# Kernel optimization log

Measured on AMD Instinct MI355X. Metric: run time of the kernel, lower is better.

Reference implementation:

```python
import jax, jax.numpy as jnp
import numpy as np

N_NODES = 50000
N_EDGES = 800000
NODE_DIM = 128
EMBED_DIM = 128


def _gcn_conv(x, W, b, src, dst):
    """GCNConv: y = D^{-1/2} (A + I) D^{-1/2} X W + b (unit edge weights)."""
    n = x.shape[0]
    xw = x @ W  # [N, out]
    loop = jnp.arange(n, dtype=src.dtype)
    src2 = jnp.concatenate([src, loop])  # self-loops appended
    dst2 = jnp.concatenate([dst, loop])
    w2 = jnp.ones(src2.shape[0], dtype=xw.dtype)
    deg = jax.ops.segment_sum(w2, dst2, num_segments=n)
    dinv = jnp.where(deg > 0, jax.lax.rsqrt(deg), jnp.zeros_like(deg))
    norm = dinv[src2] * w2 * dinv[dst2]  # [E+N]
    out = jax.ops.segment_sum(norm[:, None] * xw[src2], dst2, num_segments=n)
    return out + b


def setup_inputs() -> dict:
    key = jax.random.key(0)
    ks = jax.random.split(key, 20)
    inp = {
        'node_feat': jax.random.normal(ks[0], (N_NODES, NODE_DIM), dtype=jnp.float32),
        'src': jax.random.randint(ks[1], (N_EDGES,), 0, N_NODES, dtype=jnp.int64) if jax.config.jax_enable_x64 else jax.random.randint(ks[1], (N_EDGES,), 0, N_NODES),
        'dst': jax.random.randint(ks[2], (N_EDGES,), 0, N_NODES),
        'h': jax.random.normal(ks[3], (N_NODES, EMBED_DIM), dtype=jnp.float32),
    }
    sc_in = 1.0 / np.sqrt(NODE_DIM)
    sc_2e = 1.0 / np.sqrt(2 * EMBED_DIM)
    sc_e = 1.0 / np.sqrt(EMBED_DIM)
    # conv weight/bias + gate linear weight/bias for z, r, h gates
    for i, g in enumerate(['z', 'r', 'hh']):
        inp[f'Wc_{g}'] = jax.random.normal(ks[4 + 4 * i], (NODE_DIM, EMBED_DIM), dtype=jnp.float32) * sc_in
        inp[f'bc_{g}'] = jnp.zeros((EMBED_DIM,), dtype=jnp.float32)
        inp[f'Wl_{g}'] = jax.random.normal(ks[5 + 4 * i], (2 * EMBED_DIM, EMBED_DIM), dtype=jnp.float32) * sc_2e
        inp[f'bl_{g}'] = jnp.zeros((EMBED_DIM,), dtype=jnp.float32)
    inp['W_lin'] = jax.random.normal(ks[16], (EMBED_DIM, EMBED_DIM), dtype=jnp.float32) * sc_e
    inp['b_lin'] = jnp.zeros((EMBED_DIM,), dtype=jnp.float32)
    return inp


def reference(node_feat, src, dst, h,
              Wc_z, bc_z, Wl_z, bl_z,
              Wc_r, bc_r, Wl_r, bl_r,
              Wc_hh, bc_hh, Wl_hh, bl_hh,
              W_lin, b_lin):
    # TGCN GRU cell
    cz = _gcn_conv(node_feat, Wc_z, bc_z, src, dst)
    Z = jax.nn.sigmoid(jnp.concatenate([cz, h], axis=1) @ Wl_z + bl_z)
    cr = _gcn_conv(node_feat, Wc_r, bc_r, src, dst)
    R = jax.nn.sigmoid(jnp.concatenate([cr, h], axis=1) @ Wl_r + bl_r)
    ch = _gcn_conv(node_feat, Wc_hh, bc_hh, src, dst)
    H_tilde = jnp.tanh(jnp.concatenate([ch, h * R], axis=1) @ Wl_hh + bl_hh)
    h_0 = Z * h + (1.0 - Z) * H_tilde
    # wrapper: relu + linear
    z_out = jax.nn.relu(h_0) @ W_lin + b_lin
    return (z_out, h_0)
```

## Files before the change

kernel.cpp:

```cpp
#include <hip/hip_runtime.h>
#include <math.h>

#define NN 50000
#define DD 128
#define EE 800000
#define NSUB 3125

typedef __attribute__((ext_vector_type(8))) short short8;
typedef __attribute__((ext_vector_type(4))) float f32x4;

__device__ __forceinline__ ushort f2bf(float f) {
    union { float f; unsigned u; } v; v.f = f;
    unsigned r = v.u + 0x7FFF + ((v.u >> 16) & 1);
    return (ushort)(r >> 16);
}
__device__ __forceinline__ float bf2f(ushort u) {
    return __uint_as_float(((unsigned)u) << 16);
}
__device__ __forceinline__ float sigm(float x) { return 1.f / (1.f + expf(-x)); }

__global__ void k_cvtprep(const float* __restrict__ X, ushort* __restrict__ Xb,
                          const float* __restrict__ h, ushort* __restrict__ hb,
                          const int* __restrict__ dste, int* __restrict__ deg,
                          const float* __restrict__ Wc_z, const float* __restrict__ Wl_z,
                          const float* __restrict__ bc_z, const float* __restrict__ bl_z,
                          const float* __restrict__ Wc_r, const float* __restrict__ Wl_r,
                          const float* __restrict__ bc_r, const float* __restrict__ bl_r,
                          const float* __restrict__ Wc_h, const float* __restrict__ Wl_h,
                          const float* __restrict__ bc_h, const float* __restrict__ bl_h,
                          const float* __restrict__ W_lin,
                          ushort* __restrict__ WAs, ushort* __restrict__ WBs,
                          ushort* __restrict__ WLs, float* __restrict__ bA,
                          float* __restrict__ bB) {
    if (blockIdx.x < 6250) {
        int i = blockIdx.x * 256 + threadIdx.x;
        float4 v = ((const float4*)X)[i];
        ushort4 u;
        u.x = f2bf(v.x); u.y = f2bf(v.y); u.z = f2bf(v.z); u.w = f2bf(v.w);
        ((ushort4*)Xb)[i] = u;
        if (i < EE) atomicAdd(&deg[dste[i]], 1);
        return;
    }
    if (blockIdx.x < 12500) {
        int i = (blockIdx.x - 6250) * 256 + threadIdx.x;
        float4 v = ((const float4*)h)[i];
        ushort4 u;
        u.x = f2bf(v.x); u.y = f2bf(v.y); u.z = f2bf(v.z); u.w = f2bf(v.w);
        ((ushort4*)hb)[i] = u;
        return;
    }
    int idx = (blockIdx.x - 12500) * 256 + threadIdx.x;
    if (idx < 65536) {
        int k = idx >> 8, c = idx & 255, cc = c & 127;
        const float* Wc = (c < 128) ? Wc_z : Wc_r;
        const float* Wl = (c < 128) ? Wl_z : Wl_r;
        float v;
        if (k < 128) {
            float s = 0.f;
            for (int j = 0; j < 128; j++) s += Wc[k * 128 + j] * Wl[j * 128 + cc];
            v = s;
        } else {
            v = Wl[k * 128 + cc];
        }
        WAs[(k >> 5) * 8192 + (c >> 4) * 512 + (((k >> 3) & 3) * 16 + (c & 15)) * 8 + (k & 7)] = f2bf(v);
    } else if (idx < 98304) {
        int i2 = idx - 65536;
        int k = i2 >> 7, c = i2 & 127;
        float v;
        if (k < 128) {
            float s = 0.f;
            for (int j = 0; j < 128; j++) s += Wc_h[k * 128 + j] * Wl_h[j * 128 + c];
            v = s;
        } else {
            v = Wl_h[k * 128 + c];
        }
        WBs[(k >> 5) * 4096 + (c >> 4) * 512 + (((k >> 3) & 3) * 16 + (c & 15)) * 8 + (k & 7)] = f2bf(v);
    } else if (idx < 114688) {
        int i3 = idx - 98304;
        int k = i3 >> 7, c = i3 & 127;
        WLs[(k >> 5) * 4096 + (c >> 4) * 512 + (((k >> 3) & 3) * 16 + (c & 15)) * 8 + (k & 7)] = f2bf(W_lin[k * 128 + c]);
    } else if (idx < 114944) {
        int c = idx - 114688, cc = c & 127;
        const float* bc = (c < 128) ? bc_z : bc_r;
        const float* Wl = (c < 128) ? Wl_z : Wl_r;
        const float* bl = (c < 128) ? bl_z : bl_r;
        float s = bl[cc];
        for (int j = 0; j < 128; j++) s += bc[j] * Wl[j * 128 + cc];
        bA[c] = s;
    } else if (idx < 115072) {
        int c = idx - 114944;
        float s = bl_h[c];
        for (int j = 0; j < 128; j++) s += bc_h[j] * Wl_h[j * 128 + c];
        bB[c] = s;
    }
}

__global__ void k_alloc(const int* __restrict__ deg, int* __restrict__ off,
                        int* __restrict__ cur, int* __restrict__ cursor,
                        float* __restrict__ dinv) {
    int n = blockIdx.x * 256 + threadIdx.x;
    int lane = threadIdx.x & 63;
    int d = (n < NN) ? deg[n] : 0;
    int x = d;
    #pragma unroll
    for (int o = 1; o < 64; o <<= 1) {
        int y = __shfl_up(x, o);
        if (lane >= o) x += y;
    }
    int total = __shfl(x, 63);
    int base = 0;
    if (lane == 0) base = atomicAdd(cursor, total);
    base = __shfl(base, 0);
    if (n < NN) {
        int o2 = base + x - d;
        off[n] = o2;
        cur[n] = o2;
        dinv[n] = rsqrtf((float)d + 1.0f);
    }
}

__global__ void k_fill(const int* __restrict__ src, const int* __restrict__ dst,
                       int* __restrict__ cur, int* __restrict__ csr) {
    int e = blockIdx.x * 256 + threadIdx.x;
    if (e < EE) {
        int slot = atomicAdd(&cur[dst[e]], 1);
        csr[slot] = src[e];
    }
}

__global__ __launch_bounds__(256) void k_gather(const ushort* __restrict__ Xb,
                                                const int* __restrict__ csr,
                                                const int* __restrict__ off,
                                                const int* __restrict__ deg,
                                                const float* __restrict__ dinv,
                                                ushort* __restrict__ AXb) {
    int tid = blockIdx.x * 256 + threadIdx.x;
    int n = tid >> 6, lane = tid & 63;
    if (n >= NN) return;
    int o   = __builtin_amdgcn_readfirstlane(off[n]);
    int cnt = __builtin_amdgcn_readfirstlane(deg[n]);
    float dd = dinv[n];
    uint a = *((const uint*)(Xb + (size_t)n * 128 + lane * 2));
    float acc0 = dd * dd * __uint_as_float(a << 16);
    float acc1 = dd * dd * __uint_as_float(a & 0xffff0000u);
    int i = 0;
    for (; i + 8 <= cnt; i += 8) {
        int s[8];
        #pragma unroll
        for (int u = 0; u < 8; u++) s[u] = csr[o + i + u];
        uint v[8];
        #pragma unroll
        for (int u = 0; u < 8; u++) v[u] = *((const uint*)(Xb + (size_t)s[u] * 128 + lane * 2));
        float c[8];
        #pragma unroll
        for (int u = 0; u < 8; u++) c[u] = dinv[s[u]] * dd;
        #pragma unroll
        for (int u = 0; u < 8; u++) {
            acc0 += c[u] * __uint_as_float(v[u] << 16);
            acc1 += c[u] * __uint_as_float(v[u] & 0xffff0000u);
        }
    }
    for (; i < cnt; i++) {
        int s = csr[o + i];
        float c = dinv[s] * dd;
        uint v = *((const uint*)(Xb + (size_t)s * 128 + lane * 2));
        acc0 += c * __uint_as_float(v << 16);
        acc1 += c * __uint_as_float(v & 0xffff0000u);
    }
    ushort2 u2; u2.x = f2bf(acc0); u2.y = f2bf(acc1);
    *((ushort2*)(AXb + (size_t)n * 128 + lane * 2)) = u2;
}

__global__ __launch_bounds__(256, 2) void k_gemmA(const ushort* __restrict__ AXb,
                                                  const ushort* __restrict__ hb,
                                                  const float* __restrict__ h,
                                                  const ushort* __restrict__ WAs,
                                                  const float* __restrict__ bA,
                                                  ushort* __restrict__ Zt,
                                                  ushort* __restrict__ hRb) {
    __shared__ ushort scr[4][1024];
    const int tid = threadIdx.x, lane = tid & 63, w = tid >> 6;
    const int tx = lane & 15, g = lane >> 4;

    short8 wf[4][8];
    #pragma unroll
    for (int ct = 0; ct < 4; ct++)
        #pragma unroll
        for (int ks = 0; ks < 8; ks++)
            wf[ct][ks] = *((const short8*)(WAs + ks * 8192 + (w * 4 + ct) * 512 + lane * 8));
    float bias[4];
    #pragma unroll
    for (int ct = 0; ct < 4; ct++) bias[ct] = bA[w * 64 + ct * 16 + tx];

    for (int rs = blockIdx.x; rs < NSUB; rs += gridDim.x) {
        const int arow = rs * 16 + tx;
        short8 axf[4], hf[4];
        #pragma unroll
        for (int ks = 0; ks < 4; ks++) {
            axf[ks] = *((const short8*)(AXb + (size_t)arow * 128 + ks * 32 + g * 8));
            hf[ks]  = *((const short8*)(hb  + (size_t)arow * 128 + ks * 32 + g * 8));
        }
        f32x4 acc[4];
        #pragma unroll
        for (int ct = 0; ct < 4; ct++) acc[ct] = (f32x4){0.f, 0.f, 0.f, 0.f};
        #pragma unroll
        for (int ks = 0; ks < 4; ks++)
            #pragma unroll
            for (int ct = 0; ct < 4; ct++)
                acc[ct] = __builtin_amdgcn_mfma_f32_16x16x32_bf16(axf[ks], wf[ct][ks], acc[ct], 0, 0, 0);
        #pragma unroll
        for (int ks = 0; ks < 4; ks++)
            #pragma unroll
            for (int ct = 0; ct < 4; ct++)
                acc[ct] = __builtin_amdgcn_mfma_f32_16x16x32_bf16(hf[ks], wf[ct][4 + ks], acc[ct], 0, 0, 0);

        const int r0 = rs * 16 + g * 4;
        if (w < 2) {
            #pragma unroll
            for (int ct = 0; ct < 4; ct++) {
                int col = w * 64 + ct * 16 + tx;
                ushort4 z4;
                z4.x = f2bf(sigm(acc[ct][0] + bias[ct]));
                z4.y = f2bf(sigm(acc[ct][1] + bias[ct]));
                z4.z = f2bf(sigm(acc[ct][2] + bias[ct]));
                z4.w = f2bf(sigm(acc[ct][3] + bias[ct]));
                *((ushort4*)(Zt + (size_t)col * NN + r0)) = z4;
            }
        } else {
            #pragma unroll
            for (int ct = 0; ct < 4; ct++) {
                int cl = ct * 16 + tx;
                int cc = (w - 2) * 64 + cl;
                #pragma unroll
                for (int r = 0; r < 4; r++) {
                    float hval = h[(size_t)(r0 + r) * 128 + cc];
                    float R = sigm(acc[ct][r] + bias[ct]);
                    scr[w][(g * 4 + r) * 64 + cl] = f2bf(hval * R);
                }
            }
            int c0 = lane, c1 = lane + 64;
            short8 t0 = *((const short8*)(&scr[w][(c0 >> 3) * 64 + (c0 & 7) * 8]));
            short8 t1 = *((const short8*)(&scr[w][(c1 >> 3) * 64 + (c1 & 7) * 8]));
            *((short8*)(hRb + (size_t)(rs * 16 + (c0 >> 3)) * 128 + (w - 2) * 64 + (c0 & 7) * 8)) = t0;
            *((short8*)(hRb + (size_t)(rs * 16 + (c1 >> 3)) * 128 + (w - 2) * 64 + (c1 & 7) * 8)) = t1;
        }
    }
}

__global__ __launch_bounds__(256, 2) void k_gemmB(const ushort* __restrict__ AXb,
                                                  const ushort* __restrict__ hRb,
                                                  const float* __restrict__ h,
                                                  const ushort* __restrict__ Zt,
                                                  const ushort* __restrict__ WBs,
                                                  const float* __restrict__ bB,
                                                  float* __restrict__ out_h,
                                                  ushort* __restrict__ rl) {
    __shared__ float scrf[4][512];
    const int tid = threadIdx.x, lane = tid & 63, w = tid >> 6;
    const int tx = lane & 15, g = lane >> 4;

    short8 wf[2][8];
    #pragma unroll
    for (int ct = 0; ct < 2; ct++)
        #pragma unroll
        for (int ks = 0; ks < 8; ks++)
            wf[ct][ks] = *((const short8*)(WBs + ks * 4096 + (w * 2 + ct) * 512 + lane * 8));
    float bias[2];
    #pragma unroll
    for (int ct = 0; ct < 2; ct++) bias[ct] = bB[w * 32 + ct * 16 + tx];

    for (int rs = blockIdx.x; rs < NSUB; rs += gridDim.x) {
        const int arow = rs * 16 + tx;
        short8 axf[4], hrf[4];
        #pragma unroll
        for (int ks = 0; ks < 4; ks++) {
            axf[ks] = *((const short8*)(AXb + (size_t)arow * 128 + ks * 32 + g * 8));
            hrf[ks] = *((const short8*)(hRb + (size_t)arow * 128 + ks * 32 + g * 8));
        }
        f32x4 acc[2];
        #pragma unroll
        for (int ct = 0; ct < 2; ct++) acc[ct] = (f32x4){0.f, 0.f, 0.f, 0.f};
        #pragma unroll
        for (int ks = 0; ks < 4; ks++)
            #pragma unroll
            for (int ct = 0; ct < 2; ct++)
                acc[ct] = __builtin_amdgcn_mfma_f32_16x16x32_bf16(axf[ks], wf[ct][ks], acc[ct], 0, 0, 0);
        #pragma unroll
        for (int ks = 0; ks < 4; ks++)
            #pragma unroll
            for (int ct = 0; ct < 2; ct++)
                acc[ct] = __builtin_amdgcn_mfma_f32_16x16x32_bf16(hrf[ks], wf[ct][4 + ks], acc[ct], 0, 0, 0);

        const int r0 = rs * 16 + g * 4;
        #pragma unroll
        for (int ct = 0; ct < 2; ct++) {
            int col = w * 32 + ct * 16 + tx;
            ushort4 z4 = *((const ushort4*)(Zt + (size_t)col * NN + r0));
            float zz[4] = {bf2f(z4.x), bf2f(z4.y), bf2f(z4.z), bf2f(z4.w)};
            #pragma unroll
            for (int r = 0; r < 4; r++) {
                float hval = h[(size_t)(r0 + r) * 128 + col];
                float H = tanhf(acc[ct][r] + bias[ct]);
                float h0 = zz[r] * hval + (1.f - zz[r]) * H;
                scrf[w][(g * 4 + r) * 32 + ct * 16 + tx] = h0;
            }
        }
        int row = lane >> 2, cb = (lane & 3) * 8;
        float4 h0a = *((const float4*)(&scrf[w][row * 32 + cb]));
        float4 h0b = *((const float4*)(&scrf[w][row * 32 + cb + 4]));
        size_t go = (size_t)(rs * 16 + row) * 128 + w * 32 + cb;
        *((float4*)(out_h + go)) = h0a;
        *((float4*)(out_h + go + 4)) = h0b;
        short8 rv;
        rv[0] = (short)f2bf(fmaxf(h0a.x, 0.f)); rv[1] = (short)f2bf(fmaxf(h0a.y, 0.f));
        rv[2] = (short)f2bf(fmaxf(h0a.z, 0.f)); rv[3] = (short)f2bf(fmaxf(h0a.w, 0.f));
        rv[4] = (short)f2bf(fmaxf(h0b.x, 0.f)); rv[5] = (short)f2bf(fmaxf(h0b.y, 0.f));
        rv[6] = (short)f2bf(fmaxf(h0b.z, 0.f)); rv[7] = (short)f2bf(fmaxf(h0b.w, 0.f));
        *((short8*)(rl + go)) = rv;
    }
}

__global__ __launch_bounds__(256, 4) void k_gemmC(const ushort* __restrict__ rl,
                                                  const ushort* __restrict__ WLs,
                                                  const float* __restrict__ b_lin,
                                                  float* __restrict__ out_z) {
    const int tid = threadIdx.x, lane = tid & 63, w = tid >> 6;
    const int tx = lane & 15, g = lane >> 4;

    short8 wf[2][4];
    #pragma unroll
    for (int ct = 0; ct < 2; ct++)
        #pragma unroll
        for (int ks = 0; ks < 4; ks++)
            wf[ct][ks] = *((const short8*)(WLs + ks * 4096 + (w * 2 + ct) * 512 + lane * 8));
    float bias[2];
    #pragma unroll
    for (int ct = 0; ct < 2; ct++) bias[ct] = b_lin[w * 32 + ct * 16 + tx];

    for (int rs = blockIdx.x; rs < NSUB; rs += gridDim.x) {
        const int arow = rs * 16 + tx;
        short8 rlf[4];
        #pragma unroll
        for (int ks = 0; ks < 4; ks++)
            rlf[ks] = *((const short8*)(rl + (size_t)arow * 128 + ks * 32 + g * 8));
        f32x4 acc[2];
        #pragma unroll
        for (int ct = 0; ct < 2; ct++) acc[ct] = (f32x4){0.f, 0.f, 0.f, 0.f};
        #pragma unroll
        for (int ks = 0; ks < 4; ks++)
            #pragma unroll
            for (int ct = 0; ct < 2; ct++)
                acc[ct] = __builtin_amdgcn_mfma_f32_16x16x32_bf16(rlf[ks], wf[ct][ks], acc[ct], 0, 0, 0);

        const int r0 = rs * 16 + g * 4;
        #pragma unroll
        for (int ct = 0; ct < 2; ct++) {
            int col = w * 32 + ct * 16 + tx;
            #pragma unroll
            for (int r = 0; r < 4; r++)
                out_z[(size_t)(r0 + r) * 128 + col] = acc[ct][r] + bias[ct];
        }
    }
}


extern "C" void kernel_launch(void* const* d_in, const int* in_sizes, int n_in,
                              void* d_out, int out_size, void* d_ws, size_t ws_size,
                              hipStream_t stream) {
    const float* X    = (const float*)d_in[0];
    const int*   src  = (const int*)d_in[1];
    const int*   dst  = (const int*)d_in[2];
    const float* h    = (const float*)d_in[3];
    const float* Wc_z = (const float*)d_in[4];
    const float* bc_z = (const float*)d_in[5];
    const float* Wl_z = (const float*)d_in[6];
    const float* bl_z = (const float*)d_in[7];
    const float* Wc_r = (const float*)d_in[8];
    const float* bc_r = (const float*)d_in[9];
    const float* Wl_r = (const float*)d_in[10];
    const float* bl_r = (const float*)d_in[11];
    const float* Wc_h = (const float*)d_in[12];
    const float* bc_h = (const float*)d_in[13];
    const float* Wl_h = (const float*)d_in[14];
    const float* bl_h = (const float*)d_in[15];
    const float* W_lin = (const float*)d_in[16];
    const float* b_lin = (const float*)d_in[17];

    float* out_z = (float*)d_out;
    float* out_h = out_z + (size_t)NN * DD;

    float* ws = (float*)d_ws;
    float*  dinv   = ws;
    int*    deg    = (int*)(ws + 50048);
    int*    cur    = (int*)(ws + 100096);
    int*    cursor = (int*)(ws + 150144);
    int*    off    = (int*)(ws + 150208);
    int*    csr    = (int*)(ws + 200256);
    float*  bA     = ws + 1000320;
    float*  bB     = ws + 1000576;
    ushort* WAs    = (ushort*)(ws + 1000704);
    ushort* WBs    = (ushort*)(ws + 1033472);
    ushort* WLs    = (ushort*)(ws + 1049856);
    ushort* AXb    = (ushort*)(ws + 1058048);
    ushort* Xb     = (ushort*)(ws + 4258048);
    ushort* Zt     = Xb;
    ushort* hb     = (ushort*)(ws + 7458048);
    ushort* rl     = hb;
    ushort* hRb    = (ushort*)(ws + 10658048);

    hipMemsetAsync(deg, 0, 100160 * sizeof(int), stream);
    k_cvtprep<<<12950, 256, 0, stream>>>(X, Xb, h, hb, dst, deg,
                                         Wc_z, Wl_z, bc_z, bl_z, Wc_r, Wl_r, bc_r, bl_r,
                                         Wc_h, Wl_h, bc_h, bl_h, W_lin,
                                         WAs, WBs, WLs, bA, bB);
    k_alloc<<<196, 256, 0, stream>>>(deg, off, cur, cursor, dinv);
    k_fill<<<3125, 256, 0, stream>>>(src, dst, cur, csr);
    k_gather<<<12500, 256, 0, stream>>>(Xb, csr, off, deg, dinv, AXb);
    k_gemmA<<<512, 256, 0, stream>>>(AXb, hb, h, WAs, bA, Zt, hRb);
    k_gemmB<<<512, 256, 0, stream>>>(AXb, hRb, h, Zt, WBs, bB, out_h, rl);
    k_gemmC<<<1024, 256, 0, stream>>>(rl, WLs, b_lin, out_z);
}
```

Baseline: 327.3 us.

## Fuse final linear into gate GEMM and convert h to bf16 on the fly

Drops the separate h-to-bf16 conversion pass; gemmA now reads fp32 h directly and converts it in registers. The relu+linear output GEMM is fused into gemmB: relu(h0) goes to a swizzled shared-memory tile and a second MFMA pass produces out_z, so the rl intermediate no longer round-trips through global memory and one launch is removed. The prep kernel becomes grid-strided with far fewer blocks. In exchange, gemmBC holds more weight registers and adds two block barriers per row tile, which may lower occupancy.

```diff
diff --git a/kernel.cpp b/kernel.cpp
--- a/kernel.cpp
+++ b/kernel.cpp
@@ -19,37 +19,34 @@
 }
 __device__ __forceinline__ float sigm(float x) { return 1.f / (1.f + expf(-x)); }
 
-__global__ void k_cvtprep(const float* __restrict__ X, ushort* __restrict__ Xb,
-                          const float* __restrict__ h, ushort* __restrict__ hb,
-                          const int* __restrict__ dste, int* __restrict__ deg,
-                          const float* __restrict__ Wc_z, const float* __restrict__ Wl_z,
-                          const float* __restrict__ bc_z, const float* __restrict__ bl_z,
-                          const float* __restrict__ Wc_r, const float* __restrict__ Wl_r,
-                          const float* __restrict__ bc_r, const float* __restrict__ bl_r,
-                          const float* __restrict__ Wc_h, const float* __restrict__ Wl_h,
-                          const float* __restrict__ bc_h, const float* __restrict__ bl_h,
-                          const float* __restrict__ W_lin,
-                          ushort* __restrict__ WAs, ushort* __restrict__ WBs,
-                          ushort* __restrict__ WLs, float* __restrict__ bA,
-                          float* __restrict__ bB) {
-    if (blockIdx.x < 6250) {
-        int i = blockIdx.x * 256 + threadIdx.x;
-        float4 v = ((const float4*)X)[i];
-        ushort4 u;
-        u.x = f2bf(v.x); u.y = f2bf(v.y); u.z = f2bf(v.z); u.w = f2bf(v.w);
-        ((ushort4*)Xb)[i] = u;
-        if (i < EE) atomicAdd(&deg[dste[i]], 1);
+__global__ void k_pre(const float* __restrict__ X, ushort* __restrict__ Xb,
+                      const int* __restrict__ dste, int* __restrict__ deg,
+                      const float* __restrict__ Wc_z, const float* __restrict__ Wl_z,
+                      const float* __restrict__ bc_z, const float* __restrict__ bl_z,
+                      const float* __restrict__ Wc_r, const float* __restrict__ Wl_r,
+                      const float* __restrict__ bc_r, const float* __restrict__ bl_r,
+                      const float* __restrict__ Wc_h, const float* __restrict__ Wl_h,
+                      const float* __restrict__ bc_h, const float* __restrict__ bl_h,
+                      const float* __restrict__ W_lin,
+                      ushort* __restrict__ WAs, ushort* __restrict__ WBs,
+                      ushort* __restrict__ WLs, float* __restrict__ bA,
+                      float* __restrict__ bB) {
+    if (blockIdx.x < 1024) {
+        const int stride = 1024 * 256;
+        int t0 = blockIdx.x * 256 + threadIdx.x;
+        #pragma unroll 2
+        for (int i = t0; i < 1600000; i += stride) {
+            float4 v = ((const float4*)X)[i];
+            ushort4 u;
+            u.x = f2bf(v.x); u.y = f2bf(v.y); u.z = f2bf(v.z); u.w = f2bf(v.w);
+            ((ushort4*)Xb)[i] = u;
+        }
+        #pragma unroll 2
+        for (int e = t0; e < EE; e += stride)
+            atomicAdd(&deg[dste[e]], 1);
         return;
     }
-    if (blockIdx.x < 12500) {
-        int i = (blockIdx.x - 6250) * 256 + threadIdx.x;
-        float4 v = ((const float4*)h)[i];
-        ushort4 u;
-        u.x = f2bf(v.x); u.y = f2bf(v.y); u.z = f2bf(v.z); u.w = f2bf(v.w);
-        ((ushort4*)hb)[i] = u;
-        return;
-    }
-    int idx = (blockIdx.x - 12500) * 256 + threadIdx.x;
+    int idx = (blockIdx.x - 1024) * 256 + threadIdx.x;
     if (idx < 65536) {
         int k = idx >> 8, c = idx & 255, cc = c & 127;
         const float* Wc = (c < 128) ? Wc_z : Wc_r;
@@ -57,6 +54,7 @@
         float v;
         if (k < 128) {
             float s = 0.f;
+            #pragma unroll 8
             for (int j = 0; j < 128; j++) s += Wc[k * 128 + j] * Wl[j * 128 + cc];
             v = s;
         } else {
@@ -69,6 +67,7 @@
         float v;
         if (k < 128) {
             float s = 0.f;
+            #pragma unroll 8
             for (int j = 0; j < 128; j++) s += Wc_h[k * 128 + j] * Wl_h[j * 128 + c];
             v = s;
         } else {
@@ -85,11 +84,13 @@
         const float* Wl = (c < 128) ? Wl_z : Wl_r;
         const float* bl = (c < 128) ? bl_z : bl_r;
         float s = bl[cc];
+        #pragma unroll 8
         for (int j = 0; j < 128; j++) s += bc[j] * Wl[j * 128 + cc];
         bA[c] = s;
     } else if (idx < 115072) {
         int c = idx - 114944;
         float s = bl_h[c];
+        #pragma unroll 8
         for (int j = 0; j < 128; j++) s += bc_h[j] * Wl_h[j * 128 + c];
         bB[c] = s;
     }
@@ -172,7 +173,6 @@
 }
 
 __global__ __launch_bounds__(256, 2) void k_gemmA(const ushort* __restrict__ AXb,
-                                                  const ushort* __restrict__ hb,
                                                   const float* __restrict__ h,
                                                   const ushort* __restrict__ WAs,
                                                   const float* __restrict__ bA,
@@ -196,9 +196,21 @@
         const int arow = rs * 16 + tx;
         short8 axf[4], hf[4];
         #pragma unroll
-        for (int ks = 0; ks < 4; ks++) {
+        for (int ks = 0; ks < 4; ks++)
             axf[ks] = *((const short8*)(AXb + (size_t)arow * 128 + ks * 32 + g * 8));
-            hf[ks]  = *((const short8*)(hb  + (size_t)arow * 128 + ks * 32 + g * 8));
+        {
+            const float4* hp = (const float4*)(h + (size_t)arow * 128);
+            #pragma unroll
+            for (int ks = 0; ks < 4; ks++) {
+                float4 u0 = hp[ks * 8 + g * 2];
+                float4 u1 = hp[ks * 8 + g * 2 + 1];
+                short8 tt;
+                tt[0] = (short)f2bf(u0.x); tt[1] = (short)f2bf(u0.y);
+                tt[2] = (short)f2bf(u0.z); tt[3] = (short)f2bf(u0.w);
+                tt[4] = (short)f2bf(u1.x); tt[5] = (short)f2bf(u1.y);
+                tt[6] = (short)f2bf(u1.z); tt[7] = (short)f2bf(u1.w);
+                hf[ks] = tt;
+            }
         }
         f32x4 acc[4];
         #pragma unroll
@@ -247,27 +259,37 @@
     }
 }
 
-__global__ __launch_bounds__(256, 2) void k_gemmB(const ushort* __restrict__ AXb,
-                                                  const ushort* __restrict__ hRb,
-                                                  const float* __restrict__ h,
-                                                  const ushort* __restrict__ Zt,
-                                                  const ushort* __restrict__ WBs,
-                                                  const float* __restrict__ bB,
-                                                  float* __restrict__ out_h,
-                                                  ushort* __restrict__ rl) {
+__global__ __launch_bounds__(256, 2) void k_gemmBC(const ushort* __restrict__ AXb,
+                                                   const ushort* __restrict__ hRb,
+                                                   const float* __restrict__ h,
+                                                   const ushort* __restrict__ Zt,
+                                                   const ushort* __restrict__ WBs,
+                                                   const ushort* __restrict__ WLs,
+                                                   const float* __restrict__ bB,
+                                                   const float* __restrict__ b_lin,
+                                                   float* __restrict__ out_h,
+                                                   float* __restrict__ out_z) {
     __shared__ float scrf[4][512];
+    __shared__ ushort rlt[2048];
     const int tid = threadIdx.x, lane = tid & 63, w = tid >> 6;
     const int tx = lane & 15, g = lane >> 4;
 
-    short8 wf[2][8];
+    short8 wfB[2][8], wfL[2][4];
     #pragma unroll
-    for (int ct = 0; ct < 2; ct++)
+    for (int ct = 0; ct < 2; ct++) {
         #pragma unroll
         for (int ks = 0; ks < 8; ks++)
-            wf[ct][ks] = *((const short8*)(WBs + ks * 4096 + (w * 2 + ct) * 512 + lane * 8));
-    float bias[2];
+            wfB[ct][ks] = *((const short8*)(WBs + ks * 4096 + (w * 2 + ct) * 512 + lane * 8));
+        #pragma unroll
+        for (int ks = 0; ks < 4; ks++)
+            wfL[ct][ks] = *((const short8*)(WLs + ks * 4096 + (w * 2 + ct) * 512 + lane * 8));
+    }
+    float biasB[2], biasL[2];
     #pragma unroll
-    for (int ct = 0; ct < 2; ct++) bias[ct] = bB[w * 32 + ct * 16 + tx];
+    for (int ct = 0; ct < 2; ct++) {
+        biasB[ct] = bB[w * 32 + ct * 16 + tx];
+        biasL[ct] = b_lin[w * 32 + ct * 16 + tx];
+    }
 
     for (int rs = blockIdx.x; rs < NSUB; rs += gridDim.x) {
         const int arow = rs * 16 + tx;
@@ -284,12 +306,12 @@
         for (int ks = 0; ks < 4; ks++)
             #pragma unroll
             for (int ct = 0; ct < 2; ct++)
-                acc[ct] = __builtin_amdgcn_mfma_f32_16x16x32_bf16(axf[ks], wf[ct][ks], acc[ct], 0, 0, 0);
+                acc[ct] = __builtin_amdgcn_mfma_f32_16x16x32_bf16(axf[ks], wfB[ct][ks], acc[ct], 0, 0, 0);
         #pragma unroll
         for (int ks = 0; ks < 4; ks++)
             #pragma unroll
             for (int ct = 0; ct < 2; ct++)
-                acc[ct] = __builtin_amdgcn_mfma_f32_16x16x32_bf16(hrf[ks], wf[ct][4 + ks], acc[ct], 0, 0, 0);
+                acc[ct] = __builtin_amdgcn_mfma_f32_16x16x32_bf16(hrf[ks], wfB[ct][4 + ks], acc[ct], 0, 0, 0);
 
         const int r0 = rs * 16 + g * 4;
         #pragma unroll
@@ -300,66 +322,41 @@
             #pragma unroll
             for (int r = 0; r < 4; r++) {
                 float hval = h[(size_t)(r0 + r) * 128 + col];
-                float H = tanhf(acc[ct][r] + bias[ct]);
+                float H = tanhf(acc[ct][r] + biasB[ct]);
                 float h0 = zz[r] * hval + (1.f - zz[r]) * H;
                 scrf[w][(g * 4 + r) * 32 + ct * 16 + tx] = h0;
+                int rr = g * 4 + r;
+                *((ushort*)((char*)rlt + rr * 256 + ((col * 2) ^ ((rr & 7) << 4)))) = f2bf(fmaxf(h0, 0.f));
             }
         }
-        int row = lane >> 2, cb = (lane & 3) * 8;
-        float4 h0a = *((const float4*)(&scrf[w][row * 32 + cb]));
-        float4 h0b = *((const float4*)(&scrf[w][row * 32 + cb + 4]));
-        size_t go = (size_t)(rs * 16 + row) * 128 + w * 32 + cb;
-        *((float4*)(out_h + go)) = h0a;
-        *((float4*)(out_h + go + 4)) = h0b;
-        short8 rv;
-        rv[0] = (short)f2bf(fmaxf(h0a.x, 0.f)); rv[1] = (short)f2bf(fmaxf(h0a.y, 0.f));
-        rv[2] = (short)f2bf(fmaxf(h0a.z, 0.f)); rv[3] = (short)f2bf(fmaxf(h0a.w, 0.f));
-        rv[4] = (short)f2bf(fmaxf(h0b.x, 0.f)); rv[5] = (short)f2bf(fmaxf(h0b.y, 0.f));
-        rv[6] = (short)f2bf(fmaxf(h0b.z, 0.f)); rv[7] = (short)f2bf(fmaxf(h0b.w, 0.f));
-        *((short8*)(rl + go)) = rv;
-    }
-}
-
-__global__ __launch_bounds__(256, 4) void k_gemmC(const ushort* __restrict__ rl,
-                                                  const ushort* __restrict__ WLs,
-                                                  const float* __restrict__ b_lin,
-                                                  float* __restrict__ out_z) {
-    const int tid = threadIdx.x, lane = tid & 63, w = tid >> 6;
-    const int tx = lane & 15, g = lane >> 4;
-
-    short8 wf[2][4];
-    #pragma unroll
-    for (int ct = 0; ct < 2; ct++)
-        #pragma unroll
-        for (int ks = 0; ks < 4; ks++)
-            wf[ct][ks] = *((const short8*)(WLs + ks * 4096 + (w * 2 + ct) * 512 + lane * 8));
-    float bias[2];
-    #pragma unroll
-    for (int ct = 0; ct < 2; ct++) bias[ct] = b_lin[w * 32 + ct * 16 + tx];
-
-    for (int rs = blockIdx.x; rs < NSUB; rs += gridDim.x) {
-        const int arow = rs * 16 + tx;
-        short8 rlf[4];
-        #pragma unroll
-        for (int ks = 0; ks < 4; ks++)
-            rlf[ks] = *((const short8*)(rl + (size_t)arow * 128 + ks * 32 + g * 8));
-        f32x4 acc[2];
-        #pragma unroll
-        for (int ct = 0; ct < 2; ct++) acc[ct] = (f32x4){0.f, 0.f, 0.f, 0.f};
-        #pragma unroll
-        for (int ks = 0; ks < 4; ks++)
+        {
+            int row = lane >> 2, cb = (lane & 3) * 8;
+            float4 h0a = *((const float4*)(&scrf[w][row * 32 + cb]));
+            float4 h0b = *((const float4*)(&scrf[w][row * 32 + cb + 4]));
+            size_t go = (size_t)(rs * 16 + row) * 128 + w * 32 + cb;
+            *((float4*)(out_h + go)) = h0a;
+            *((float4*)(out_h + go + 4)) = h0b;
+        }
+        __syncthreads();
+
+        f32x4 accC[2];
+        #pragma unroll
+        for (int ct = 0; ct < 2; ct++) accC[ct] = (f32x4){0.f, 0.f, 0.f, 0.f};
+        #pragma unroll
+        for (int ks = 0; ks < 4; ks++) {
+            short8 a = *((const short8*)((const char*)rlt + tx * 256 + ((ks * 64 + g * 16) ^ ((tx & 7) << 4))));
             #pragma unroll
             for (int ct = 0; ct < 2; ct++)
-                acc[ct] = __builtin_amdgcn_mfma_f32_16x16x32_bf16(rlf[ks], wf[ct][ks], acc[ct], 0, 0, 0);
-
-        const int r0 = rs * 16 + g * 4;
+                accC[ct] = __builtin_amdgcn_mfma_f32_16x16x32_bf16(a, wfL[ct][ks], accC[ct], 0, 0, 0);
+        }
         #pragma unroll
         for (int ct = 0; ct < 2; ct++) {
             int col = w * 32 + ct * 16 + tx;
             #pragma unroll
             for (int r = 0; r < 4; r++)
-                out_z[(size_t)(r0 + r) * 128 + col] = acc[ct][r] + bias[ct];
-        }
+                out_z[(size_t)(r0 + r) * 128 + col] = accC[ct][r] + biasL[ct];
+        }
+        __syncthreads();
     }
 }
 
@@ -404,19 +401,16 @@
     ushort* AXb    = (ushort*)(ws + 1058048);
     ushort* Xb     = (ushort*)(ws + 4258048);
     ushort* Zt     = Xb;
-    ushort* hb     = (ushort*)(ws + 7458048);
-    ushort* rl     = hb;
-    ushort* hRb    = (ushort*)(ws + 10658048);
+    ushort* hRb    = (ushort*)(ws + 7458048);
 
     hipMemsetAsync(deg, 0, 100160 * sizeof(int), stream);
-    k_cvtprep<<<12950, 256, 0, stream>>>(X, Xb, h, hb, dst, deg,
-                                         Wc_z, Wl_z, bc_z, bl_z, Wc_r, Wl_r, bc_r, bl_r,
-                                         Wc_h, Wl_h, bc_h, bl_h, W_lin,
-                                         WAs, WBs, WLs, bA, bB);
+    k_pre<<<1474, 256, 0, stream>>>(X, Xb, dst, deg,
+                                    Wc_z, Wl_z, bc_z, bl_z, Wc_r, Wl_r, bc_r, bl_r,
+                                    Wc_h, Wl_h, bc_h, bl_h, W_lin,
+                                    WAs, WBs, WLs, bA, bB);
     k_alloc<<<196, 256, 0, stream>>>(deg, off, cur, cursor, dinv);
     k_fill<<<3125, 256, 0, stream>>>(src, dst, cur, csr);
     k_gather<<<12500, 256, 0, stream>>>(Xb, csr, off, deg, dinv, AXb);
-    k_gemmA<<<512, 256, 0, stream>>>(AXb, hb, h, WAs, bA, Zt, hRb);
-    k_gemmB<<<512, 256, 0, stream>>>(AXb, hRb, h, Zt, WBs, bB, out_h, rl);
-    k_gemmC<<<1024, 256, 0, stream>>>(rl, WLs, b_lin, out_z);
-}
+    k_gemmA<<<512, 256, 0, stream>>>(AXb, h, WAs, bA, Zt, hRb);
+    k_gemmBC<<<512, 256, 0, stream>>>(AXb, hRb, h, Zt, WBs, WLs, bB, b_lin, out_h, out_z);
+}
```

Result: faster. 316.0 us (-3.4%).
